# Optimization experiments

Measured on AMD Instinct MI355X. Metric: run time of the kernel, lower is better.

The kernel has to match this reference:

```python
import jax, jax.numpy as jnp
import numpy as np
from jax import lax

C_IN = 128; RED = 4; NH = 4; G = 2; KU = 3; RANGE = 11.0; SCALE_F = 2
HID = C_IN // RED           # 32  hidden_dim
GC = HID // G               # 16  group_channel
HD = HID // NH              # 8   per-head q/k dim (== attn_dim)
VD = C_IN // NH             # 32  per-head v dim
SCALE = float((C_IN // (RED * NH)) ** -0.5)
EPS = 1e-6


def _ln_ch(x, w, b):
    # channel-first LayerNorm over dim 1 (matches torch module's non-channels-last branch)
    u = x.mean(1, keepdims=True)
    s = ((x - u) ** 2).mean(1, keepdims=True)
    return w[None, :, None, None] * ((x - u) * lax.rsqrt(s + EPS)) + b[None, :, None, None]


def _resize_ac(x, oh, ow):
    # bilinear resize, align_corners=True (separable gather)
    B, Cc, H, W = x.shape
    ys = jnp.arange(oh, dtype=x.dtype) * ((H - 1) / (oh - 1))
    xs = jnp.arange(ow, dtype=x.dtype) * ((W - 1) / (ow - 1))
    y0 = jnp.floor(ys).astype(jnp.int32); y1 = jnp.minimum(y0 + 1, H - 1)
    x0 = jnp.floor(xs).astype(jnp.int32); x1 = jnp.minimum(x0 + 1, W - 1)
    wy = (ys - y0)[None, None, :, None]
    wx = (xs - x0)[None, None, None, :]
    t = x[:, :, y0, :] * (1 - wy) + x[:, :, y1, :] * wy
    return t[:, :, :, x0] * (1 - wx) + t[:, :, :, x1] * wx


def _grid_sample(img, grid):
    # torch.grid_sample: bilinear, padding_mode='zeros', align_corners=True
    # img (N,C,H,W), grid (N,Hg,Wg,2) in (x,y) order, range [-1,1]
    N, Cc, H, W = img.shape
    ix = (grid[..., 0] + 1.0) * 0.5 * (W - 1)
    iy = (grid[..., 1] + 1.0) * 0.5 * (H - 1)
    x0f = jnp.floor(ix); y0f = jnp.floor(iy)
    wx = ix - x0f; wy = iy - y0f
    x0 = x0f.astype(jnp.int32); x1 = x0 + 1
    y0 = y0f.astype(jnp.int32); y1 = y0 + 1

    def corner(yi, xi, w):
        valid = (yi >= 0) & (yi < H) & (xi >= 0) & (xi < W)
        yc = jnp.clip(yi, 0, H - 1); xc = jnp.clip(xi, 0, W - 1)
        vals = jax.vmap(lambda im, yy, xx: im[:, yy, xx])(img, yc, xc)  # (N,C,Hg,Wg)
        return jnp.where(valid[:, None], vals, 0.0) * w[:, None]

    return (corner(y0, x0, (1 - wy) * (1 - wx)) + corner(y0, x1, (1 - wy) * wx)
            + corner(y1, x0, wy * (1 - wx)) + corner(y1, x1, wy * wx))


def _forward(x, ln_w, ln_b, wq, wk, dw_w, oln_w, oln_b, off_w, off_b, rpb_table):
    B, C, H, W = x.shape
    oh, ow = H * SCALE_F, W * SCALE_F
    v = x
    xn = _ln_ch(x, ln_w, ln_b)
    q = jnp.einsum('oc,bchw->bohw', wq, xn)
    k = jnp.einsum('oc,bchw->bohw', wk, xn)
    q = _resize_ac(q, oh, ow)                                    # (B,HID,oh,ow)

    # offset prediction (grouped)
    qoff = q.reshape(B * G, GC, oh, ow)
    dn = ('NCHW', 'OIHW', 'NCHW')
    t = lax.conv_general_dilated(qoff, dw_w, (1, 1), ((1, 1), (1, 1)),
                                 dimension_numbers=dn, feature_group_count=GC)
    t = _ln_ch(t, oln_w, oln_b)
    t = t * jax.nn.sigmoid(t)                                    # SiLU
    pred = lax.conv_general_dilated(t, off_w, (1, 1), ((1, 1), (1, 1)),
                                    dimension_numbers=dn) + off_b[None, :, None, None]
    base = jnp.arange(-(KU // 2), KU // 2 + 1, dtype=x.dtype)
    base_off = jnp.stack([jnp.repeat(base, KU), jnp.tile(base, KU)], 1).reshape(1, 2 * KU * KU, 1, 1)
    off = jnp.tanh(pred) * RANGE + base_off                      # (BG, 2*9, oh, ow)

    # get_offset: (kh kw d) channel layout -> absolute normalized grid
    off = off.reshape(B * G, KU, KU, 2, oh, ow).transpose(0, 1, 4, 2, 5, 3)  # (BG,kh,oh,kw,ow,2)
    rows = jnp.arange(oh, dtype=x.dtype); cols = jnp.arange(ow, dtype=x.dtype)
    idx = jnp.stack(jnp.meshgrid(rows, cols, indexing='ij'), -1)  # (oh,ow,2) = (row,col)
    off = off + idx.reshape(1, 1, oh, 1, ow, 2)
    grid = off.reshape(B * G, KU * oh, KU * ow, 2)
    gy = 2 * grid[..., 0] / (oh - 1) - 1
    gx = 2 * grid[..., 1] / (ow - 1) - 1
    grid = jnp.stack([gx, gy], -1)                               # flip to (x,y)

    kf = _grid_sample(k.reshape(B * G, HID // G, H, W), grid)    # (BG,cg,3oh,3ow)
    vf = _grid_sample(v.reshape(B * G, C // G, H, W), grid)

    def to_heads(f, ch):
        # (BG,ch,KU*oh,KU*ow) -> (B,NH,oh*ow,KU*KU,G*ch//NH)
        f = f.reshape(B, G, ch, KU, oh, KU, ow)
        f = f.transpose(0, 4, 6, 3, 5, 1, 2).reshape(B, oh * ow, KU * KU, G * ch)
        f = f.reshape(B, oh * ow, KU * KU, NH, G * ch // NH).transpose(0, 3, 1, 2, 4)
        return f

    kh = to_heads(kf, HID // G) + rpb_table                      # (B,NH,N1,9,HD)
    vh = to_heads(vf, C // G)                                    # (B,NH,N1,9,VD)
    qh = q.reshape(B, NH, HD, oh * ow).transpose(0, 1, 3, 2) * SCALE  # (B,NH,N1,HD)

    attn = jnp.einsum('bhnc,bhnkc->bhnk', qh, kh)
    attn = jax.nn.softmax(attn, axis=-1)
    out = jnp.einsum('bhnk,bhnkc->bhnc', attn, vh)               # (B,NH,N1,VD)
    return out.transpose(0, 1, 3, 2).reshape(B, C, oh, ow)


def setup_inputs() -> dict:
    key = jax.random.key(0)
    ks = jax.random.split(key, 6)
    B, H, W = 4, 64, 64
    x = jax.random.normal(ks[0], (B, C_IN, H, W), jnp.float32)
    return {
        'x': x,
        'ln_w': jnp.ones((C_IN,), jnp.float32),
        'ln_b': jnp.zeros((C_IN,), jnp.float32),
        'wq': jax.random.normal(ks[1], (HID, C_IN), jnp.float32) / np.sqrt(C_IN).astype(np.float32),
        'wk': jax.random.normal(ks[2], (HID, C_IN), jnp.float32) / np.sqrt(C_IN).astype(np.float32),
        'dw_w': jax.random.normal(ks[3], (GC, 1, 3, 3), jnp.float32) / 3.0,
        'oln_w': jnp.ones((GC,), jnp.float32),
        'oln_b': jnp.zeros((GC,), jnp.float32),
        'off_w': jax.random.normal(ks[4], (2 * KU * KU, GC, 3, 3), jnp.float32) * 0.02,
        'off_b': jnp.zeros((2 * KU * KU,), jnp.float32),
        'rpb_table': jax.random.normal(ks[5], (1, NH, 1, KU * KU, HD), jnp.float32) * 0.02,
    }


def reference(x, ln_w, ln_b, wq, wk, dw_w, oln_w, oln_b, off_w, off_b, rpb_table):
    return _forward(x, ln_w, ln_b, wq, wk, dw_w, oln_w, oln_b, off_w, off_b, rpb_table)
```

## Files before the change

kernel.cpp:

```cpp
#include <hip/hip_runtime.h>
#include <hip/hip_fp16.h>
#include <cstdint>
#include <cstddef>

#define DEV __device__ __forceinline__

namespace {

constexpr float SCALE  = 0.35355339059327373f;
constexpr float RATIO  = 63.0f / 127.0f;
constexpr float RANGEF = 11.0f;
constexpr float EPS    = 1e-6f;

typedef _Float16 h2 __attribute__((ext_vector_type(2)));

DEV float fdot2(h2 a, h2 b, float c) { return __builtin_amdgcn_fdot2(a, b, c, false); }
DEV h2 pkrtz(float a, float b) {
  auto r = __builtin_amdgcn_cvt_pkrtz(a, b);
  union { decltype(r) i; h2 o; } u; u.i = r; return u.o;
}
DEV h2 permh(unsigned a, unsigned b, unsigned sel) {
  unsigned r = __builtin_amdgcn_perm(a, b, sel);
  union { unsigned u; h2 h; } u; u.u = r; return u.h;
}
DEV void fax(float4& a, float s, const float4& b) {
  a.x = fmaf(s, b.x, a.x); a.y = fmaf(s, b.y, a.y);
  a.z = fmaf(s, b.z, a.z); a.w = fmaf(s, b.w, a.w);
}

DEV void corners(float iy, float ix, float* wc, int* idx) {
  float yf = floorf(iy), xf = floorf(ix);
  float wy = iy - yf, wx = ix - xf;
  int y0 = (int)yf, x0 = (int)xf;
  #pragma unroll
  for (int c = 0; c < 4; ++c) {
    int yy = y0 + (c >> 1), xx = x0 + (c & 1);
    bool valid = ((unsigned)yy < 64u) && ((unsigned)xx < 64u);
    float w = ((c >> 1) ? wy : 1.f - wy) * ((c & 1) ? wx : 1.f - wx);
    wc[c] = valid ? w : 0.f;
    idx[c] = valid ? yy * 64 + xx : 0;
  }
}

__global__ __launch_bounds__(256) void k_transpose(
    const float* __restrict__ x, __half* __restrict__ vH,
    const float* __restrict__ offw, const float* __restrict__ dww,
    const float* __restrict__ wq, const float* __restrict__ wk,
    const float* __restrict__ rpb,
    h2* __restrict__ wT2H, float* __restrict__ dwT,
    h2* __restrict__ wqH, h2* __restrict__ wkH, h2* __restrict__ rpbH) {
  if (blockIdx.x == 0) {
    for (int idx = threadIdx.x; idx < 1296; idx += 256) {
      int t2 = idx / 72, r = idx % 72, j2 = r / 9, i = r % 9;
      int tap = t2 >> 1, h = t2 & 1;
      int o = h * 9 + i;
      wT2H[idx] = pkrtz(offw[o * 144 + (2 * j2) * 9 + tap],
                        offw[o * 144 + (2 * j2 + 1) * 9 + tap]);
    }
    for (int idx = threadIdx.x; idx < 144; idx += 256) {
      int j = idx / 9, tap = idx % 9;
      dwT[tap * 16 + j] = dww[idx];
    }
    for (int idx = threadIdx.x; idx < 2048; idx += 256) {
      int c2 = idx >> 5, o = idx & 31;
      wqH[idx] = pkrtz(wq[o * 128 + 2 * c2], wq[o * 128 + 2 * c2 + 1]);
      wkH[idx] = pkrtz(wk[o * 128 + 2 * c2], wk[o * 128 + 2 * c2 + 1]);
    }
    for (int idx = threadIdx.x; idx < 144; idx += 256) {
      int row = idx >> 2, j = idx & 3;
      rpbH[idx] = pkrtz(rpb[row * 8 + 2 * j], rpb[row * 8 + 2 * j + 1]);
    }
  }
  __shared__ float tile[128 * 65];
  int b = blockIdx.x >> 6, y = blockIdx.x & 63;
  const float* xp = x + (size_t)b * 128 * 4096 + (size_t)y * 64;
  int xc = threadIdx.x & 63, cb = threadIdx.x >> 6;
  #pragma unroll
  for (int i = 0; i < 32; ++i) {
    int c = cb * 32 + i;
    tile[c * 65 + xc] = xp[(size_t)c * 4096 + xc];
  }
  __syncthreads();
  int p = threadIdx.x >> 2, c0 = (threadIdx.x & 3) * 32;
  __half* op = vH + ((size_t)b * 4096 + (size_t)y * 64 + p) * 128 + c0;
  #pragma unroll
  for (int i = 0; i < 32; i += 8) {
    union { float4 f; __half2 h[4]; } u;
    #pragma unroll
    for (int j = 0; j < 4; ++j)
      u.h[j] = __floats2half2_rn(tile[(c0 + i + 2 * j) * 65 + p],
                                 tile[(c0 + i + 2 * j + 1) * 65 + p]);
    *(float4*)(op + i) = u.f;
  }
}

__global__ __launch_bounds__(256) void k_lnproj(
    const float* __restrict__ x, const float* __restrict__ lnw,
    const float* __restrict__ lnb, const h2* __restrict__ wqH,
    const h2* __restrict__ wkH, float* __restrict__ qT,
    __half* __restrict__ kH) {
  int tid = blockIdx.x * 256 + threadIdx.x;
  int pos = tid >> 4, o4 = tid & 15;
  int b = pos >> 12, sp = pos & 4095;
  const float* xp = x + (size_t)b * 524288 + sp;

  float s = 0.f, ss = 0.f;
  #pragma unroll
  for (int i = 0; i < 8; ++i) {
    float v = xp[(size_t)(o4 * 8 + i) * 4096];
    s += v; ss = fmaf(v, v, ss);
  }
  #pragma unroll
  for (int m = 1; m < 16; m <<= 1) {
    s += __shfl_xor(s, m);
    ss += __shfl_xor(ss, m);
  }
  float mean = s * (1.f / 128.f);
  float rstd = rsqrtf(ss * (1.f / 128.f) - mean * mean + EPS);

  int isk = o4 >> 3;
  const h2* w = (isk ? wkH : wqH) + (o4 & 7) * 4;
  float a0 = 0.f, a1 = 0.f, a2 = 0.f, a3 = 0.f;
  #pragma unroll 4
  for (int c2 = 0; c2 < 64; ++c2) {
    float v0 = xp[(size_t)(2 * c2) * 4096];
    float v1 = xp[(size_t)(2 * c2 + 1) * 4096];
    float xn0 = (v0 - mean) * rstd * lnw[2 * c2] + lnb[2 * c2];
    float xn1 = (v1 - mean) * rstd * lnw[2 * c2 + 1] + lnb[2 * c2 + 1];
    h2 xh = pkrtz(xn0, xn1);
    const h2* wr = w + c2 * 32;
    a0 = fdot2(xh, wr[0], a0); a1 = fdot2(xh, wr[1], a1);
    a2 = fdot2(xh, wr[2], a2); a3 = fdot2(xh, wr[3], a3);
  }
  if (!isk) {
    *(float4*)(qT + (size_t)pos * 32 + (o4 & 7) * 4) = make_float4(a0, a1, a2, a3);
  } else {
    union { uint2 u; __half2 h[2]; } o;
    o.h[0] = __floats2half2_rn(a0, a1);
    o.h[1] = __floats2half2_rn(a2, a3);
    *(uint2*)(kH + (size_t)pos * 32 + (o4 & 7) * 4) = o.u;
  }
}

__global__ __launch_bounds__(256) void k_resize(const float* __restrict__ qT,
                                                float* __restrict__ qrT) {
  int tid = blockIdx.x * 256 + threadIdx.x;
  int pos = tid >> 2, q4 = tid & 3;
  int b = pos >> 14, rem = pos & 16383;
  int oy = rem >> 7, ox = rem & 127;
  float ys = oy * RATIO, xs = ox * RATIO;
  float yf = floorf(ys), xf = floorf(xs);
  int y0 = (int)yf, x0 = (int)xf;
  int y1 = min(y0 + 1, 63), x1 = min(x0 + 1, 63);
  float wy = ys - yf, wx = xs - xf;
  const float4* p00 = (const float4*)(qT + ((size_t)b * 4096 + y0 * 64 + x0) * 32 + q4 * 8);
  const float4* p01 = (const float4*)(qT + ((size_t)b * 4096 + y0 * 64 + x1) * 32 + q4 * 8);
  const float4* p10 = (const float4*)(qT + ((size_t)b * 4096 + y1 * 64 + x0) * 32 + q4 * 8);
  const float4* p11 = (const float4*)(qT + ((size_t)b * 4096 + y1 * 64 + x1) * 32 + q4 * 8);
  float w00 = (1.f - wy) * (1.f - wx), w01 = (1.f - wy) * wx;
  float w10 = wy * (1.f - wx), w11 = wy * wx;
  float4* op = (float4*)(qrT + (size_t)pos * 32 + q4 * 8);
  #pragma unroll
  for (int i = 0; i < 2; ++i) {
    float4 r = {0.f, 0.f, 0.f, 0.f};
    fax(r, w00, p00[i]); fax(r, w01, p01[i]);
    fax(r, w10, p10[i]); fax(r, w11, p11[i]);
    op[i] = r;
  }
}

__global__ __launch_bounds__(256) void k_dwln(
    const float* __restrict__ qrT, const float* __restrict__ dwT,
    const float* __restrict__ olnw, const float* __restrict__ olnb,
    __half* __restrict__ tH) {
  int tid = blockIdx.x * 256 + threadIdx.x;
  int pos = tid >> 2, sub = tid & 3;
  int b = pos >> 14, rem = pos & 16383;
  int oy = rem >> 7, ox = rem & 127;
  int h8 = sub & 1;
  float4 a0 = {}, a1 = {};
  #pragma unroll
  for (int kh = 0; kh < 3; ++kh) {
    int ty = oy + kh - 1;
    if ((unsigned)ty >= 128u) continue;
    #pragma unroll
    for (int kw = 0; kw < 3; ++kw) {
      int tx = ox + kw - 1;
      if ((unsigned)tx >= 128u) continue;
      int tap = kh * 3 + kw;
      const float4* p =
          (const float4*)(qrT + ((size_t)b * 16384 + (size_t)ty * 128 + tx) * 32 + sub * 8);
      const float* dw = dwT + tap * 16 + h8 * 8;
      float4 v0 = p[0], v1 = p[1];
      a0.x = fmaf(dw[0], v0.x, a0.x); a0.y = fmaf(dw[1], v0.y, a0.y);
      a0.z = fmaf(dw[2], v0.z, a0.z); a0.w = fmaf(dw[3], v0.w, a0.w);
      a1.x = fmaf(dw[4], v1.x, a1.x); a1.y = fmaf(dw[5], v1.y, a1.y);
      a1.z = fmaf(dw[6], v1.z, a1.z); a1.w = fmaf(dw[7], v1.w, a1.w);
    }
  }
  float s = a0.x + a0.y + a0.z + a0.w + a1.x + a1.y + a1.z + a1.w;
  float ss = a0.x * a0.x + a0.y * a0.y + a0.z * a0.z + a0.w * a0.w +
             a1.x * a1.x + a1.y * a1.y + a1.z * a1.z + a1.w * a1.w;
  s += __shfl_xor(s, 1);
  ss += __shfl_xor(ss, 1);
  float mean = s * (1.f / 16.f);
  float rstd = rsqrtf(ss * (1.f / 16.f) - mean * mean + EPS);
  const float* ow = olnw + h8 * 8;
  const float* ob = olnb + h8 * 8;
  float r[8] = {a0.x, a0.y, a0.z, a0.w, a1.x, a1.y, a1.z, a1.w};
  #pragma unroll
  for (int i = 0; i < 8; ++i) {
    float t = (r[i] - mean) * rstd * ow[i] + ob[i];
    r[i] = t / (1.f + expf(-t));
  }
  union { uint4 u; h2 h[4]; } o_;
  o_.h[0] = pkrtz(r[0], r[1]); o_.h[1] = pkrtz(r[2], r[3]);
  o_.h[2] = pkrtz(r[4], r[5]); o_.h[3] = pkrtz(r[6], r[7]);
  *(uint4*)(tH + (size_t)pos * 32 + sub * 8) = o_.u;
}

__global__ __launch_bounds__(256) void k_off(
    const __half* __restrict__ tH, const h2* __restrict__ wT2H,
    const float* __restrict__ offb, float* __restrict__ crd) {
  int tid = blockIdx.x * 128 + (threadIdx.x & 127);
  int h = __builtin_amdgcn_readfirstlane(threadIdx.x >> 7);
  int bg = tid >> 14, rem = tid & 16383;
  int oy = rem >> 7, ox = rem & 127;
  int b = bg >> 1, g = bg & 1;

  float a[9];
  #pragma unroll
  for (int i = 0; i < 9; ++i) a[i] = 0.f;

  #pragma unroll
  for (int kh = 0; kh < 3; ++kh) {
    int ty = oy + kh - 1;
    if (ty < 0 || ty >= 128) continue;
    const __half* base = tH + ((size_t)b * 16384 + (size_t)ty * 128) * 32 + g * 16;
    #pragma unroll
    for (int kw = 0; kw < 3; ++kw) {
      int tap = kh * 3 + kw;
      int tx = ox + kw - 1;
      if ((unsigned)tx >= 128u) continue;
      union { uint4 u[2]; h2 hh[8]; } in;
      const uint4* p = (const uint4*)(base + (size_t)tx * 32);
      in.u[0] = p[0]; in.u[1] = p[1];
      const h2* wrow = wT2H + (size_t)(tap * 2 + h) * 72;
      #pragma unroll
      for (int j2 = 0; j2 < 8; ++j2) {
        h2 f = in.hh[j2];
        #pragma unroll
        for (int i = 0; i < 9; ++i)
          a[i] = fdot2(f, wrow[j2 * 9 + i], a[i]);
      }
    }
  }

  const float* bb = offb + h * 9;
  float* cp = crd + (size_t)tid * 18 + h * 9;
  #pragma unroll
  for (int i = 0; i < 9; ++i) {
    int o = h * 9 + i;
    int kp = o >> 1;
    float basec = (o & 1) ? (float)(kp % 3 - 1 + ox) : (float)(kp / 3 - 1 + oy);
    cp[i] = fmaf(tanhf(a[i] + bb[i]), RANGEF, basec) * RATIO;
  }
}

__global__ __launch_bounds__(256) void k_attn2(
    const float* __restrict__ qrT, const __half* __restrict__ kH,
    const __half* __restrict__ vH, const float* __restrict__ crd,
    const h2* __restrict__ rpbH, float* __restrict__ out) {
  __shared__ h2 qh2S[256];
  __shared__ float crdS[576];
  __shared__ __align__(16) float4 corn4[576];
  __shared__ float lgS[576];
  int b = blockIdx.x >> 10;
  int p0 = (blockIdx.x & 1023) * 16;
  const h2* kbase = (const h2*)(kH + (size_t)b * 131072);

  {
    int pp = threadIdx.x >> 4, j = threadIdx.x & 15;
    float2 qv = *(const float2*)(qrT + ((size_t)b * 16384 + p0 + pp) * 32 + j * 2);
    qh2S[threadIdx.x] = pkrtz(qv.x * SCALE, qv.y * SCALE);
    if (threadIdx.x < 144) {
      int g = threadIdx.x / 72, i = threadIdx.x - (threadIdx.x / 72) * 72;
      const float4* src = (const float4*)(crd + ((size_t)(b * 2 + g) * 16384 + p0) * 18);
      *(float4*)(crdS + g * 288 + i * 4) = src[i];
    }
  }

  if (threadIdx.x < 32) {
    int pl = threadIdx.x >> 1, g = threadIdx.x & 1;
    float2 cc = *(const float2*)(crd +
        ((size_t)(b * 2 + g) * 16384 + p0 + pl) * 18 + 16);
    float wc[4]; int idx[4];
    corners(cc.x, cc.y, wc, idx);

    h2 qa[8];
    const float* qg = qrT + ((size_t)b * 16384 + p0 + pl) * 32 + g * 16;
    #pragma unroll
    for (int j = 0; j < 8; ++j) {
      float2 qv = *(const float2*)(qg + 2 * j);
      qa[j] = pkrtz(qv.x * SCALE, qv.y * SCALE);
    }
    const h2* kb = kbase + g * 8;
    float a0 = 0.f, a1 = 0.f;
    #pragma unroll
    for (int c = 0; c < 4; ++c) {
      union { float4 f[2]; h2 h[8]; } kk;
      const float4* kr = (const float4*)(kb + (size_t)idx[c] * 16);
      kk.f[0] = kr[0]; kk.f[1] = kr[1];
      float d0 = 0.f, d1 = 0.f;
      #pragma unroll
      for (int j = 0; j < 4; ++j) {
        d0 = fdot2(qa[j], kk.h[j], d0);
        d1 = fdot2(qa[4 + j], kk.h[4 + j], d1);
      }
      a0 = fmaf(wc[c], d0, a0);
      a1 = fmaf(wc[c], d1, a1);
    }
    const h2* rp0 = rpbH + (2 * g * 9 + 8) * 4;
    const h2* rp1 = rpbH + ((2 * g + 1) * 9 + 8) * 4;
    #pragma unroll
    for (int j = 0; j < 4; ++j) {
      a0 = fdot2(qa[j], rp0[j], a0);
      a1 = fdot2(qa[4 + j], rp1[j], a1);
    }
    lgS[(pl * 4 + 2 * g) * 9 + 8] = a0;
    lgS[(pl * 4 + 2 * g + 1) * 9 + 8] = a1;
    corn4[((pl * 2 + g) * 9 + 8) * 2 + 0] =
        make_float4(wc[0], __int_as_float(idx[0]), wc[1], __int_as_float(idx[1]));
    corn4[((pl * 2 + g) * 9 + 8) * 2 + 1] =
        make_float4(wc[2], __int_as_float(idx[2]), wc[3], __int_as_float(idx[3]));
  }
  __syncthreads();

  {
    int pl = threadIdx.x >> 4, r = threadIdx.x & 15;
    int g = r >> 3, kp = r & 7;
    float iy = crdS[g * 288 + pl * 18 + 2 * kp];
    float ix = crdS[g * 288 + pl * 18 + 2 * kp + 1];
    float wc[4]; int idx[4];
    corners(iy, ix, wc, idx);

    const h2* qa = qh2S + pl * 16 + g * 8;
    const h2* kb = kbase + g * 8;
    float a0 = 0.f, a1 = 0.f;
    #pragma unroll
    for (int c = 0; c < 4; ++c) {
      union { float4 f[2]; h2 h[8]; } kk;
      const float4* kr = (const float4*)(kb + (size_t)idx[c] * 16);
      kk.f[0] = kr[0]; kk.f[1] = kr[1];
      float d0 = 0.f, d1 = 0.f;
      #pragma unroll
      for (int j = 0; j < 4; ++j) {
        d0 = fdot2(qa[j], kk.h[j], d0);
        d1 = fdot2(qa[4 + j], kk.h[4 + j], d1);
      }
      a0 = fmaf(wc[c], d0, a0);
      a1 = fmaf(wc[c], d1, a1);
    }
    const h2* rp0 = rpbH + (2 * g * 9 + kp) * 4;
    const h2* rp1 = rpbH + ((2 * g + 1) * 9 + kp) * 4;
    #pragma unroll
    for (int j = 0; j < 4; ++j) {
      a0 = fdot2(qa[j], rp0[j], a0);
      a1 = fdot2(qa[4 + j], rp1[j], a1);
    }
    lgS[(pl * 4 + 2 * g) * 9 + kp] = a0;
    lgS[(pl * 4 + 2 * g + 1) * 9 + kp] = a1;
    corn4[((pl * 2 + g) * 9 + kp) * 2 + 0] =
        make_float4(wc[0], __int_as_float(idx[0]), wc[1], __int_as_float(idx[1]));
    corn4[((pl * 2 + g) * 9 + kp) * 2 + 1] =
        make_float4(wc[2], __int_as_float(idx[2]), wc[3], __int_as_float(idx[3]));
  }
  __syncthreads();

  int pl = threadIdx.x >> 4, c8 = threadIdx.x & 15;
  int g = c8 >> 3, h = c8 >> 2, ch = c8 * 8;
  int pos = p0 + pl;

  float w9[9];
  {
    const float* l = lgS + (pl * 4 + h) * 9;
    float m = l[0];
    #pragma unroll
    for (int kp = 1; kp < 9; ++kp) m = fmaxf(m, l[kp]);
    float s = 0.f;
    #pragma unroll
    for (int kp = 0; kp < 9; ++kp) { w9[kp] = __expf(l[kp] - m); s += w9[kp]; }
    float inv = 1.f / s;
    #pragma unroll
    for (int kp = 0; kp < 9; ++kp) w9[kp] *= inv;
  }

  const __half* vb = vH + (size_t)b * 524288 + ch;
  const float4* corn = corn4 + (pl * 2 + g) * 18;
  constexpr unsigned SEL_LO = 0x01000504u, SEL_HI = 0x03020706u;

  float acc[8] = {};
  #pragma unroll
  for (int kp = 0; kp < 9; ++kp) {
    float aw = w9[kp];
    float4 ca = corn[kp * 2], cb = corn[kp * 2 + 1];
    #pragma unroll
    for (int pr = 0; pr < 2; ++pr) {
      float4 cp = pr ? cb : ca;
      h2 w01 = pkrtz(aw * cp.x, aw * cp.z);
      uint4 r0 = *(const uint4*)(vb + (size_t)__float_as_int(cp.y) * 128);
      uint4 r1 = *(const uint4*)(vb + (size_t)__float_as_int(cp.w) * 128);
      acc[0] = fdot2(w01, permh(r0.x, r1.x, SEL_LO), acc[0]);
      acc[1] = fdot2(w01, permh(r0.x, r1.x, SEL_HI), acc[1]);
      acc[2] = fdot2(w01, permh(r0.y, r1.y, SEL_LO), acc[2]);
      acc[3] = fdot2(w01, permh(r0.y, r1.y, SEL_HI), acc[3]);
      acc[4] = fdot2(w01, permh(r0.z, r1.z, SEL_LO), acc[4]);
      acc[5] = fdot2(w01, permh(r0.z, r1.z, SEL_HI), acc[5]);
      acc[6] = fdot2(w01, permh(r0.w, r1.w, SEL_LO), acc[6]);
      acc[7] = fdot2(w01, permh(r0.w, r1.w, SEL_HI), acc[7]);
    }
  }

  float* op = out + ((size_t)b * 128 + ch) * 16384 + pos;
  #pragma unroll
  for (int i = 0; i < 8; ++i) op[(size_t)i * 16384] = acc[i];
}

}

extern "C" void kernel_launch(void* const* d_in, const int* in_sizes, int n_in,
                              void* d_out, int out_size, void* d_ws, size_t ws_size,
                              hipStream_t stream) {
  const float* x    = (const float*)d_in[0];
  const float* lnw  = (const float*)d_in[1];
  const float* lnb  = (const float*)d_in[2];
  const float* wq   = (const float*)d_in[3];
  const float* wk   = (const float*)d_in[4];
  const float* dww  = (const float*)d_in[5];
  const float* olnw = (const float*)d_in[6];
  const float* olnb = (const float*)d_in[7];
  const float* offw = (const float*)d_in[8];
  const float* offb = (const float*)d_in[9];
  const float* rpb  = (const float*)d_in[10];
  float* outp = (float*)d_out;

  int B = in_sizes[0] / (128 * 64 * 64);
  size_t nb = (size_t)B * 4096;
  size_t np = (size_t)B * 16384;

  char* w8 = (char*)d_ws;
  __half* vH  = (__half*)w8;  w8 += nb * 128 * 2;
  __half* kH  = (__half*)w8;  w8 += nb * 32 * 2;
  float*  qT  = (float*)w8;   w8 += nb * 32 * 4;
  float*  qrT = (float*)w8;   w8 += np * 32 * 4;
  __half* tH  = (__half*)w8;  w8 += np * 32 * 2;
  float*  crd = (float*)w8;   w8 += np * 2 * 18 * 4;
  float*  dwT = (float*)w8;   w8 += 144 * 4;
  h2*     wqH = (h2*)w8;      w8 += 2048 * 4;
  h2*     wkH = (h2*)w8;      w8 += 2048 * 4;
  h2*     wT2H= (h2*)w8;      w8 += 1296 * 4;
  h2*     rpbH= (h2*)w8;      w8 += 1024;

  hipLaunchKernelGGL(k_transpose, dim3(B * 64), dim3(256), 0, stream,
                     x, vH, offw, dww, wq, wk, rpb, wT2H, dwT, wqH, wkH, rpbH);
  hipLaunchKernelGGL(k_lnproj, dim3(B * 256), dim3(256), 0, stream,
                     x, lnw, lnb, wqH, wkH, qT, kH);
  hipLaunchKernelGGL(k_resize, dim3(B * 256), dim3(256), 0, stream, qT, qrT);
  hipLaunchKernelGGL(k_dwln, dim3(B * 256), dim3(256), 0, stream,
                     qrT, dwT, olnw, olnb, tH);
  hipLaunchKernelGGL(k_off, dim3(B * 256), dim3(256), 0, stream, tH, wT2H, offb, crd);
  hipLaunchKernelGGL(k_attn2, dim3(B * 1024), dim3(256), 0, stream,
                     qrT, kH, vH, crd, rpbH, outp);
}
```

Baseline: 107.8 us.

## Store upsampled q in fp16 with prescale and read LN input from fp16 transpose

The upsampled query buffer is now stored as pre-scaled fp16 instead of fp32, which halves its write and read traffic in the resize, depthwise-conv and attention kernels and removes the repeated scale-and-convert in attention. The LayerNorm/projection kernel now reads the already-transposed fp16 copy of x, with contiguous 256-byte rows per position, instead of strided fp32 reads from x. The cost is some precision loss: LN statistics are computed from fp16-rounded inputs and the depthwise conv consumes fp16 q. Each of the 16 threads per position now also recomputes the full 128-channel sum instead of sharing it through shuffles, and holds all 128 values in registers.

```diff
diff --git a/kernel.cpp b/kernel.cpp
--- a/kernel.cpp
+++ b/kernel.cpp
@@ -95,25 +95,24 @@
 }
 
 __global__ __launch_bounds__(256) void k_lnproj(
-    const float* __restrict__ x, const float* __restrict__ lnw,
+    const __half* __restrict__ vH, const float* __restrict__ lnw,
     const float* __restrict__ lnb, const h2* __restrict__ wqH,
     const h2* __restrict__ wkH, float* __restrict__ qT,
     __half* __restrict__ kH) {
   int tid = blockIdx.x * 256 + threadIdx.x;
   int pos = tid >> 4, o4 = tid & 15;
-  int b = pos >> 12, sp = pos & 4095;
-  const float* xp = x + (size_t)b * 524288 + sp;
+
+  union { uint4 u[16]; h2 h[64]; } xv;
+  const uint4* vp = (const uint4*)(vH + (size_t)pos * 128);
+  #pragma unroll
+  for (int i = 0; i < 16; ++i) xv.u[i] = vp[i];
 
   float s = 0.f, ss = 0.f;
   #pragma unroll
-  for (int i = 0; i < 8; ++i) {
-    float v = xp[(size_t)(o4 * 8 + i) * 4096];
-    s += v; ss = fmaf(v, v, ss);
-  }
-  #pragma unroll
-  for (int m = 1; m < 16; m <<= 1) {
-    s += __shfl_xor(s, m);
-    ss += __shfl_xor(ss, m);
+  for (int i = 0; i < 64; ++i) {
+    float fx = (float)xv.h[i][0], fy = (float)xv.h[i][1];
+    s += fx + fy;
+    ss = fmaf(fx, fx, fmaf(fy, fy, ss));
   }
   float mean = s * (1.f / 128.f);
   float rstd = rsqrtf(ss * (1.f / 128.f) - mean * mean + EPS);
@@ -121,10 +120,9 @@
   int isk = o4 >> 3;
   const h2* w = (isk ? wkH : wqH) + (o4 & 7) * 4;
   float a0 = 0.f, a1 = 0.f, a2 = 0.f, a3 = 0.f;
-  #pragma unroll 4
+  #pragma unroll 8
   for (int c2 = 0; c2 < 64; ++c2) {
-    float v0 = xp[(size_t)(2 * c2) * 4096];
-    float v1 = xp[(size_t)(2 * c2 + 1) * 4096];
+    float v0 = (float)xv.h[c2][0], v1 = (float)xv.h[c2][1];
     float xn0 = (v0 - mean) * rstd * lnw[2 * c2] + lnb[2 * c2];
     float xn1 = (v1 - mean) * rstd * lnw[2 * c2 + 1] + lnb[2 * c2 + 1];
     h2 xh = pkrtz(xn0, xn1);
@@ -143,7 +141,7 @@
 }
 
 __global__ __launch_bounds__(256) void k_resize(const float* __restrict__ qT,
-                                                float* __restrict__ qrT) {
+                                                __half* __restrict__ qrH) {
   int tid = blockIdx.x * 256 + threadIdx.x;
   int pos = tid >> 2, q4 = tid & 3;
   int b = pos >> 14, rem = pos & 16383;
@@ -159,18 +157,24 @@
   const float4* p11 = (const float4*)(qT + ((size_t)b * 4096 + y1 * 64 + x1) * 32 + q4 * 8);
   float w00 = (1.f - wy) * (1.f - wx), w01 = (1.f - wy) * wx;
   float w10 = wy * (1.f - wx), w11 = wy * wx;
-  float4* op = (float4*)(qrT + (size_t)pos * 32 + q4 * 8);
+  float4 r[2];
   #pragma unroll
   for (int i = 0; i < 2; ++i) {
-    float4 r = {0.f, 0.f, 0.f, 0.f};
-    fax(r, w00, p00[i]); fax(r, w01, p01[i]);
-    fax(r, w10, p10[i]); fax(r, w11, p11[i]);
-    op[i] = r;
-  }
+    float4 t = {0.f, 0.f, 0.f, 0.f};
+    fax(t, w00, p00[i]); fax(t, w01, p01[i]);
+    fax(t, w10, p10[i]); fax(t, w11, p11[i]);
+    r[i] = t;
+  }
+  union { uint4 u; h2 h[4]; } o;
+  o.h[0] = pkrtz(r[0].x * SCALE, r[0].y * SCALE);
+  o.h[1] = pkrtz(r[0].z * SCALE, r[0].w * SCALE);
+  o.h[2] = pkrtz(r[1].x * SCALE, r[1].y * SCALE);
+  o.h[3] = pkrtz(r[1].z * SCALE, r[1].w * SCALE);
+  *(uint4*)(qrH + (size_t)pos * 32 + q4 * 8) = o.u;
 }
 
 __global__ __launch_bounds__(256) void k_dwln(
-    const float* __restrict__ qrT, const float* __restrict__ dwT,
+    const __half* __restrict__ qrH, const float* __restrict__ dwT,
     const float* __restrict__ olnw, const float* __restrict__ olnb,
     __half* __restrict__ tH) {
   int tid = blockIdx.x * 256 + threadIdx.x;
@@ -178,7 +182,7 @@
   int b = pos >> 14, rem = pos & 16383;
   int oy = rem >> 7, ox = rem & 127;
   int h8 = sub & 1;
-  float4 a0 = {}, a1 = {};
+  float a[8] = {};
   #pragma unroll
   for (int kh = 0; kh < 3; ++kh) {
     int ty = oy + kh - 1;
@@ -188,29 +192,30 @@
       int tx = ox + kw - 1;
       if ((unsigned)tx >= 128u) continue;
       int tap = kh * 3 + kw;
-      const float4* p =
-          (const float4*)(qrT + ((size_t)b * 16384 + (size_t)ty * 128 + tx) * 32 + sub * 8);
+      union { uint4 u; h2 h[4]; } in;
+      in.u = *(const uint4*)(qrH +
+          ((size_t)b * 16384 + (size_t)ty * 128 + tx) * 32 + sub * 8);
       const float* dw = dwT + tap * 16 + h8 * 8;
-      float4 v0 = p[0], v1 = p[1];
-      a0.x = fmaf(dw[0], v0.x, a0.x); a0.y = fmaf(dw[1], v0.y, a0.y);
-      a0.z = fmaf(dw[2], v0.z, a0.z); a0.w = fmaf(dw[3], v0.w, a0.w);
-      a1.x = fmaf(dw[4], v1.x, a1.x); a1.y = fmaf(dw[5], v1.y, a1.y);
-      a1.z = fmaf(dw[6], v1.z, a1.z); a1.w = fmaf(dw[7], v1.w, a1.w);
-    }
-  }
-  float s = a0.x + a0.y + a0.z + a0.w + a1.x + a1.y + a1.z + a1.w;
-  float ss = a0.x * a0.x + a0.y * a0.y + a0.z * a0.z + a0.w * a0.w +
-             a1.x * a1.x + a1.y * a1.y + a1.z * a1.z + a1.w * a1.w;
+      #pragma unroll
+      for (int j = 0; j < 4; ++j) {
+        a[2 * j]     = fmaf(dw[2 * j],     (float)in.h[j][0], a[2 * j]);
+        a[2 * j + 1] = fmaf(dw[2 * j + 1], (float)in.h[j][1], a[2 * j + 1]);
+      }
+    }
+  }
+  float s = 0.f, ss = 0.f;
+  #pragma unroll
+  for (int i = 0; i < 8; ++i) { s += a[i]; ss = fmaf(a[i], a[i], ss); }
   s += __shfl_xor(s, 1);
   ss += __shfl_xor(ss, 1);
   float mean = s * (1.f / 16.f);
   float rstd = rsqrtf(ss * (1.f / 16.f) - mean * mean + EPS);
   const float* ow = olnw + h8 * 8;
   const float* ob = olnb + h8 * 8;
-  float r[8] = {a0.x, a0.y, a0.z, a0.w, a1.x, a1.y, a1.z, a1.w};
+  float r[8];
   #pragma unroll
   for (int i = 0; i < 8; ++i) {
-    float t = (r[i] - mean) * rstd * ow[i] + ob[i];
+    float t = (a[i] - mean) * rstd * ow[i] + ob[i];
     r[i] = t / (1.f + expf(-t));
   }
   union { uint4 u; h2 h[4]; } o_;
@@ -268,10 +273,10 @@
 }
 
 __global__ __launch_bounds__(256) void k_attn2(
-    const float* __restrict__ qrT, const __half* __restrict__ kH,
+    const __half* __restrict__ qrH, const __half* __restrict__ kH,
     const __half* __restrict__ vH, const float* __restrict__ crd,
     const h2* __restrict__ rpbH, float* __restrict__ out) {
-  __shared__ h2 qh2S[256];
+  __shared__ __align__(16) h2 qh2S[256];
   __shared__ float crdS[576];
   __shared__ __align__(16) float4 corn4[576];
   __shared__ float lgS[576];
@@ -280,9 +285,9 @@
   const h2* kbase = (const h2*)(kH + (size_t)b * 131072);
 
   {
-    int pp = threadIdx.x >> 4, j = threadIdx.x & 15;
-    float2 qv = *(const float2*)(qrT + ((size_t)b * 16384 + p0 + pp) * 32 + j * 2);
-    qh2S[threadIdx.x] = pkrtz(qv.x * SCALE, qv.y * SCALE);
+    if (threadIdx.x < 64)
+      ((uint4*)qh2S)[threadIdx.x] =
+          ((const uint4*)(qrH + (size_t)(b * 16384 + p0) * 32))[threadIdx.x];
     if (threadIdx.x < 144) {
       int g = threadIdx.x / 72, i = threadIdx.x - (threadIdx.x / 72) * 72;
       const float4* src = (const float4*)(crd + ((size_t)(b * 2 + g) * 16384 + p0) * 18);
@@ -297,13 +302,10 @@
     float wc[4]; int idx[4];
     corners(cc.x, cc.y, wc, idx);
 
-    h2 qa[8];
-    const float* qg = qrT + ((size_t)b * 16384 + p0 + pl) * 32 + g * 16;
-    #pragma unroll
-    for (int j = 0; j < 8; ++j) {
-      float2 qv = *(const float2*)(qg + 2 * j);
-      qa[j] = pkrtz(qv.x * SCALE, qv.y * SCALE);
-    }
+    union { uint4 u[2]; h2 h[8]; } qa;
+    const uint4* qg = (const uint4*)(qrH + ((size_t)(b * 16384 + p0 + pl)) * 32 + g * 16);
+    qa.u[0] = qg[0]; qa.u[1] = qg[1];
+
     const h2* kb = kbase + g * 8;
     float a0 = 0.f, a1 = 0.f;
     #pragma unroll
@@ -314,8 +316,8 @@
       float d0 = 0.f, d1 = 0.f;
       #pragma unroll
       for (int j = 0; j < 4; ++j) {
-        d0 = fdot2(qa[j], kk.h[j], d0);
-        d1 = fdot2(qa[4 + j], kk.h[4 + j], d1);
+        d0 = fdot2(qa.h[j], kk.h[j], d0);
+        d1 = fdot2(qa.h[4 + j], kk.h[4 + j], d1);
       }
       a0 = fmaf(wc[c], d0, a0);
       a1 = fmaf(wc[c], d1, a1);
@@ -324,8 +326,8 @@
     const h2* rp1 = rpbH + ((2 * g + 1) * 9 + 8) * 4;
     #pragma unroll
     for (int j = 0; j < 4; ++j) {
-      a0 = fdot2(qa[j], rp0[j], a0);
-      a1 = fdot2(qa[4 + j], rp1[j], a1);
+      a0 = fdot2(qa.h[j], rp0[j], a0);
+      a1 = fdot2(qa.h[4 + j], rp1[j], a1);
     }
     lgS[(pl * 4 + 2 * g) * 9 + 8] = a0;
     lgS[(pl * 4 + 2 * g + 1) * 9 + 8] = a1;
@@ -452,7 +454,7 @@
   __half* vH  = (__half*)w8;  w8 += nb * 128 * 2;
   __half* kH  = (__half*)w8;  w8 += nb * 32 * 2;
   float*  qT  = (float*)w8;   w8 += nb * 32 * 4;
-  float*  qrT = (float*)w8;   w8 += np * 32 * 4;
+  __half* qrH = (__half*)w8;  w8 += np * 32 * 2;
   __half* tH  = (__half*)w8;  w8 += np * 32 * 2;
   float*  crd = (float*)w8;   w8 += np * 2 * 18 * 4;
   float*  dwT = (float*)w8;   w8 += 144 * 4;
@@ -464,11 +466,11 @@
   hipLaunchKernelGGL(k_transpose, dim3(B * 64), dim3(256), 0, stream,
                      x, vH, offw, dww, wq, wk, rpb, wT2H, dwT, wqH, wkH, rpbH);
   hipLaunchKernelGGL(k_lnproj, dim3(B * 256), dim3(256), 0, stream,
-                     x, lnw, lnb, wqH, wkH, qT, kH);
-  hipLaunchKernelGGL(k_resize, dim3(B * 256), dim3(256), 0, stream, qT, qrT);
+                     vH, lnw, lnb, wqH, wkH, qT, kH);
+  hipLaunchKernelGGL(k_resize, dim3(B * 256), dim3(256), 0, stream, qT, qrH);
   hipLaunchKernelGGL(k_dwln, dim3(B * 256), dim3(256), 0, stream,
-                     qrT, dwT, olnw, olnb, tH);
+                     qrH, dwT, olnw, olnb, tH);
   hipLaunchKernelGGL(k_off, dim3(B * 256), dim3(256), 0, stream, tH, wT2H, offb, crd);
   hipLaunchKernelGGL(k_attn2, dim3(B * 1024), dim3(256), 0, stream,
-                     qrT, kH, vH, crd, rpbH, outp);
-}
+                     qrH, kH, vH, crd, rpbH, outp);
+}
```

New measurement: 117.5 us. +9.0%, slower.
